# Kernel optimization log

Measured on AMD Instinct MI355X. Metric: run time of the kernel, lower is better.

Reference implementation:

```python
import jax, jax.numpy as jnp
import numpy as np

D, S, L, W, H, V = 64, 64, 64, 300, 300, 50000
NEG = jnp.float32(-9999999.0)


def setup_inputs() -> dict:
    key = jax.random.key(0)
    ks = jax.random.split(key, 16)
    n = lambda k, shape, s=0.05: jax.random.normal(k, shape, dtype=jnp.float32) * s
    return {
        "word_indices": jax.random.randint(ks[0], (D, S, L), 0, V),
        "E": n(ks[1], (V, W), 0.1),
        "W_sent": n(ks[2], (H, W)), "b_sent": jnp.zeros((H,), jnp.float32),
        "W_par": n(ks[3], (H, H)), "b_par": jnp.zeros((H,), jnp.float32),
        "W_ch": n(ks[4], (H, H)), "b_ch": jnp.zeros((H,), jnp.float32),
        "w_root": n(ks[5], (H,)), "b_root": jnp.zeros((), jnp.float32),
        "root_embed": n(ks[6], (H,)),
        "W_r": n(ks[7], (H, 3 * H)), "b_r": jnp.zeros((H,), jnp.float32),
        "W_cls": n(ks[8], (2, H)), "b_cls": jnp.zeros((2,), jnp.float32),
    }


def reference(word_indices, E, W_sent, b_sent, W_par, b_par, W_ch, b_ch,
              w_root, b_root, root_embed, W_r, b_r, W_cls, b_cls):
    lrelu = lambda x: jax.nn.leaky_relu(x, 0.01)
    # Ragged pad+gather stage of the original, dense here (all lengths == L)
    word_embed = E[word_indices]                 # [D,S,L,W]
    # 0.5*(X[l-1] + reverse(reverse(X))[l-1]) == X[l-1]; LSTM outputs unused in source
    x_last = word_embed[:, :, -1, :]             # [D,S,W]
    enc = lrelu(x_last @ W_sent.T + b_sent)      # [D,S,H] sentence encodings
    # Pairwise parent-child edge scores (O(S^2) dots in the original loops)
    P = lrelu(enc @ W_par.T + b_par)             # [D,S,H]
    C = lrelu(enc @ W_ch.T + b_ch)               # [D,S,H]
    A = jnp.einsum('dih,djh->dij', P, C)         # [D,S,S]
    A = jnp.where(jnp.eye(S, dtype=bool)[None], NEG, A)
    A = jax.nn.softmax(A, axis=1)                # Softmax(dim=0) per doc: over parents i
    scores = enc @ w_root + b_root               # [D,S] root scores
    fri = jax.nn.softmax(scores, axis=1)         # Softmax(dim=0) over sentences
    # ri[i] = r_embeds([enc_i, sum_k A[k,i]*enc_k + fri_i*root, enc_i*sum_k A[i,k]])
    tmp = jnp.einsum('dki,dkh->dih', A, enc)     # [D,S,H]
    agg = tmp + fri[..., None] * root_embed      # [D,S,H]
    tmp3 = enc * A.sum(axis=2, keepdims=True)    # [D,S,H]
    ri = lrelu(jnp.concatenate([enc, agg, tmp3], axis=-1) @ W_r.T + b_r)  # [D,S,H]
    final = ri.mean(axis=1)                      # [D,H]
    out = final @ W_cls.T + b_cls                # [D,2]
    return out, A, fri
```

## Files before the change

kernel.cpp:

```cpp
#include <hip/hip_runtime.h>
#include <hip/hip_bf16.h>

#define NEG_INF (-9999999.0f)

typedef __attribute__((ext_vector_type(8))) short bf16x8;
typedef __attribute__((ext_vector_type(4))) float f32x4;
typedef unsigned short us;

__device__ __forceinline__ float b2f(us u) {
  union { unsigned int i; float f; } x; x.i = ((unsigned int)u) << 16; return x.f;
}
__device__ __forceinline__ us f2b(float f) {
  union { float f; unsigned int i; } x; x.f = f;
  unsigned int r = x.i + 0x7fffu + ((x.i >> 16) & 1u);
  return (us)(r >> 16);
}
__device__ __forceinline__ float lrelu(float v) { return v > 0.f ? v : 0.01f * v; }
__device__ __forceinline__ bf16x8 ld8(const us* p) { return *reinterpret_cast<const bf16x8*>(p); }

__global__ __launch_bounds__(256) void k_prep(const int* __restrict__ wi, const float* __restrict__ E,
    const float* __restrict__ Ws, const float* __restrict__ Wp, const float* __restrict__ Wc,
    const float* __restrict__ Wr,
    us* __restrict__ Wsb, us* __restrict__ Wpb, us* __restrict__ Wcb, us* __restrict__ Wrb,
    us* __restrict__ xg, us* __restrict__ encb, us* __restrict__ Pb, us* __restrict__ Cb,
    us* __restrict__ encTb) {
  int task = blockIdx.y;
  int gid = blockIdx.x * 256 + threadIdx.x;
  const int stride = 640 * 256;
  if (task < 3) {
    const float* src = (task == 0) ? Ws : (task == 1) ? Wp : Wc;
    us* dst = (task == 0) ? Wsb : (task == 1) ? Wpb : Wcb;
    for (int i = gid; i < 304 * 320; i += stride) {
      int r = i / 320, c = i - r * 320;
      dst[i] = (r < 300 && c < 300) ? f2b(src[r * 300 + c]) : 0;
    }
  } else if (task == 3) {
    for (int i = gid; i < 304 * 928; i += stride) {
      int r = i / 928, c = i - r * 928;
      Wrb[i] = (r < 300 && c < 900) ? f2b(Wr[r * 900 + c]) : 0;
    }
  } else if (task == 4) {
    for (int i = gid; i < 4096 * 320; i += stride) {
      int r = i / 320, c = i - r * 320;
      xg[i] = (c < 300) ? f2b(E[(long)wi[r * 64 + 63] * 300 + c]) : 0;
    }
  } else if (task == 5) {
    for (int i = gid; i < 3 * 4096 * 20; i += stride) {
      int b = i / 81920, rem = i - b * 81920;
      int r = rem / 20, c = 300 + (rem - r * 20);
      us* dst = (b == 0) ? encb : (b == 1) ? Pb : Cb;
      dst[r * 320 + c] = 0;
    }
  } else {
    for (int i = gid; i < 4 * 4096; i += stride)
      encTb[300 * 4096 + i] = 0;
  }
}

__device__ __forceinline__ void stage16(const us* __restrict__ g, us* lds, int units, int t) {
  const float4* s = reinterpret_cast<const float4*>(g);
  float4* d = reinterpret_cast<float4*>(lds);
  for (int i = t; i < units; i += 256) d[i] = s[i];
}

template<int NT, int KP>
__device__ __forceinline__ void sweep_lds(const us* As, const us* __restrict__ Bb,
    int bpitch, int nt0, int lo, int q, int ksn, f32x4* acc) {
  const us* ar = As + lo * KP + 8 * q;
  const us* br[NT];
#pragma unroll
  for (int t = 0; t < NT; ++t)
    br[t] = Bb + (long)((nt0 + t) * 16 + lo) * bpitch + 8 * q;
  bf16x8 b0[NT], b1[NT], b2[NT];
#pragma unroll
  for (int t = 0; t < NT; ++t) b0[t] = ld8(br[t]);
#pragma unroll
  for (int t = 0; t < NT; ++t) b1[t] = ld8(br[t] + 32);
#pragma unroll
  for (int t = 0; t < NT; ++t) b2[t] = ld8(br[t] + 64);
  bf16x8 a0 = *reinterpret_cast<const bf16x8*>(ar);
  for (int ks = 0; ks < ksn - 3; ++ks) {
    bf16x8 a1 = *reinterpret_cast<const bf16x8*>(ar + (ks + 1) * 32);
    bf16x8 bn[NT];
#pragma unroll
    for (int t = 0; t < NT; ++t) bn[t] = ld8(br[t] + (ks + 3) * 32);
#pragma unroll
    for (int t = 0; t < NT; ++t)
      acc[t] = __builtin_amdgcn_mfma_f32_16x16x32_bf16(a0, b0[t], acc[t], 0, 0, 0);
    a0 = a1;
#pragma unroll
    for (int t = 0; t < NT; ++t) { b0[t] = b1[t]; b1[t] = b2[t]; b2[t] = bn[t]; }
  }
  {
    bf16x8 a1 = *reinterpret_cast<const bf16x8*>(ar + (ksn - 2) * 32);
#pragma unroll
    for (int t = 0; t < NT; ++t)
      acc[t] = __builtin_amdgcn_mfma_f32_16x16x32_bf16(a0, b0[t], acc[t], 0, 0, 0);
    a0 = a1;
#pragma unroll
    for (int t = 0; t < NT; ++t) b0[t] = b1[t];
  }
  {
    bf16x8 a1 = *reinterpret_cast<const bf16x8*>(ar + (ksn - 1) * 32);
#pragma unroll
    for (int t = 0; t < NT; ++t)
      acc[t] = __builtin_amdgcn_mfma_f32_16x16x32_bf16(a0, b0[t], acc[t], 0, 0, 0);
    a0 = a1;
#pragma unroll
    for (int t = 0; t < NT; ++t) b0[t] = b2[t];
  }
#pragma unroll
  for (int t = 0; t < NT; ++t)
    acc[t] = __builtin_amdgcn_mfma_f32_16x16x32_bf16(a0, b0[t], acc[t], 0, 0, 0);
}

template<int NT>
__device__ __forceinline__ void sweep(const us* __restrict__ Ab, int apitch,
    const us* __restrict__ Bb, int bpitch, int m0, int nt0, int lo, int q,
    int ks0, int ksn, f32x4* acc) {
  const us* ar = Ab + (long)(m0 + lo) * apitch + 8 * q + (long)ks0 * 32;
  const us* br[NT];
#pragma unroll
  for (int t = 0; t < NT; ++t)
    br[t] = Bb + (long)((nt0 + t) * 16 + lo) * bpitch + 8 * q + (long)ks0 * 32;
  bf16x8 a0 = ld8(ar), a1 = ld8(ar + 32);
  bf16x8 b0[NT], b1[NT];
#pragma unroll
  for (int t = 0; t < NT; ++t) b0[t] = ld8(br[t]);
#pragma unroll
  for (int t = 0; t < NT; ++t) b1[t] = ld8(br[t] + 32);
  for (int ks = 0; ks < ksn - 2; ++ks) {
    bf16x8 a2 = ld8(ar + (ks + 2) * 32);
    bf16x8 b2[NT];
#pragma unroll
    for (int t = 0; t < NT; ++t) b2[t] = ld8(br[t] + (ks + 2) * 32);
#pragma unroll
    for (int t = 0; t < NT; ++t)
      acc[t] = __builtin_amdgcn_mfma_f32_16x16x32_bf16(a0, b0[t], acc[t], 0, 0, 0);
    a0 = a1; a1 = a2;
#pragma unroll
    for (int t = 0; t < NT; ++t) { b0[t] = b1[t]; b1[t] = b2[t]; }
  }
#pragma unroll
  for (int t = 0; t < NT; ++t)
    acc[t] = __builtin_amdgcn_mfma_f32_16x16x32_bf16(a0, b0[t], acc[t], 0, 0, 0);
#pragma unroll
  for (int t = 0; t < NT; ++t)
    acc[t] = __builtin_amdgcn_mfma_f32_16x16x32_bf16(a1, b1[t], acc[t], 0, 0, 0);
}

template<int NT>
__device__ __forceinline__ void epi_bf16(const f32x4* acc, const float* __restrict__ bias,
    us* __restrict__ outb, us* __restrict__ outT,
    int m0, int nt0, int lo, int q) {
#pragma unroll
  for (int t = 0; t < NT; ++t) {
    int col = (nt0 + t) * 16 + lo;
    if (col >= 300) continue;
    float bb = bias[col];
#pragma unroll
    for (int r = 0; r < 4; ++r) {
      int row = m0 + q * 4 + r;
      us h = f2b(lrelu(acc[t][r] + bb));
      outb[(long)row * 320 + col] = h;
      if (outT) outT[(long)col * 4096 + row] = h;
    }
  }
}

__global__ __launch_bounds__(256) void k_gemm_enc(const us* __restrict__ Ab,
    const us* __restrict__ Bb, const float* __restrict__ bias,
    us* __restrict__ encb, us* __restrict__ encTb) {
  __shared__ __align__(16) us As[16 * 320];
  int t = threadIdx.x;
  int m0 = blockIdx.x * 16;
  stage16(Ab + (long)m0 * 320, As, 640, t);
  __syncthreads();
  int w = t >> 6, lane = t & 63, lo = lane & 15, q = lane >> 4;
  f32x4 z = {0.f, 0.f, 0.f, 0.f};
  if (w < 3) {
    f32x4 acc[5] = {z, z, z, z, z};
    sweep_lds<5, 320>(As, Bb, 320, w * 5, lo, q, 10, acc);
    epi_bf16<5>(acc, bias, encb, encTb, m0, w * 5, lo, q);
  } else {
    f32x4 acc[4] = {z, z, z, z};
    sweep_lds<4, 320>(As, Bb, 320, 15, lo, q, 10, acc);
    epi_bf16<4>(acc, bias, encb, encTb, m0, 15, lo, q);
  }
}

__global__ __launch_bounds__(256) void k_gemm_pc(const us* __restrict__ Ab,
    const us* __restrict__ Wpb, const us* __restrict__ Wcb,
    const float* __restrict__ bp, const float* __restrict__ bc,
    us* __restrict__ Pb, us* __restrict__ Cb) {
  __shared__ __align__(16) us As[16 * 320];
  int which = blockIdx.y;
  const us* Bb = which ? Wcb : Wpb;
  const float* bias = which ? bc : bp;
  us* outb = which ? Cb : Pb;
  int t = threadIdx.x;
  int m0 = blockIdx.x * 16;
  stage16(Ab + (long)m0 * 320, As, 640, t);
  __syncthreads();
  int w = t >> 6, lane = t & 63, lo = lane & 15, q = lane >> 4;
  f32x4 z = {0.f, 0.f, 0.f, 0.f};
  if (w < 3) {
    f32x4 acc[5] = {z, z, z, z, z};
    sweep_lds<5, 320>(As, Bb, 320, w * 5, lo, q, 10, acc);
    epi_bf16<5>(acc, bias, outb, (us*)nullptr, m0, w * 5, lo, q);
  } else {
    f32x4 acc[4] = {z, z, z, z};
    sweep_lds<4, 320>(As, Bb, 320, 15, lo, q, 10, acc);
    epi_bf16<4>(acc, bias, outb, (us*)nullptr, m0, 15, lo, q);
  }
}

__global__ __launch_bounds__(256) void k_attn(
    const us* __restrict__ Pb, const us* __restrict__ Cb, const us* __restrict__ encb,
    const float* __restrict__ w_root, const float* __restrict__ b_root,
    float* __restrict__ Aout, float* __restrict__ outF,
    us* __restrict__ Atb, float* __restrict__ rsp) {
  __shared__ float Ls[64][17];
  __shared__ float pm[4][16], psum[4][16];
  __shared__ float scores[64];
  int d = blockIdx.x, jg = blockIdx.y, t = threadIdx.x;
  int w = t >> 6, lane = t & 63, lo = lane & 15, q = lane >> 4;

  if (jg == 0) {
    int rr = t >> 2, quad = t & 3;
    const us* er = encb + (long)(d * 64 + rr) * 320;
    float s = 0.f;
    for (int h = quad * 4; h + 4 <= 300; h += 16) {
      ushort4 e4 = *reinterpret_cast<const ushort4*>(er + h);
      s = fmaf(b2f(e4.x), w_root[h], s);
      s = fmaf(b2f(e4.y), w_root[h + 1], s);
      s = fmaf(b2f(e4.z), w_root[h + 2], s);
      s = fmaf(b2f(e4.w), w_root[h + 3], s);
    }
    s += __shfl_xor(s, 1);
    s += __shfl_xor(s, 2);
    if (quad == 0) scores[rr] = s + b_root[0];
    __syncthreads();
    if (t < 64) {
      float sc = scores[t];
      float m = sc;
#pragma unroll
      for (int o = 32; o > 0; o >>= 1) m = fmaxf(m, __shfl_xor(m, o, 64));
      float e = expf(sc - m);
      float sum = e;
#pragma unroll
      for (int o = 32; o > 0; o >>= 1) sum += __shfl_xor(sum, o, 64);
      outF[d * 64 + t] = e / sum;
    }
  }

  {
    const us* Pd = Pb + (long)d * 64 * 320;
    const us* Cd = Cb + (long)d * 64 * 320;
    f32x4 acc = {0.f, 0.f, 0.f, 0.f};
    sweep<1>(Pd, 320, Cd, 320, w * 16, jg, lo, q, 0, 10, &acc);
#pragma unroll
    for (int r = 0; r < 4; ++r) {
      int i = w * 16 + q * 4 + r, j = jg * 16 + lo;
      Ls[i][lo] = (i == j) ? NEG_INF : acc[r];
    }
  }
  __syncthreads();

  {
    int col = t & 15, p = t >> 4;
    if (t < 64) {
      float mx = -3.0e38f;
      for (int i = p * 16; i < p * 16 + 16; ++i) mx = fmaxf(mx, Ls[i][col]);
      pm[p][col] = mx;
    }
    __syncthreads();
    if (t < 64) {
      float gmx = fmaxf(fmaxf(pm[0][col], pm[1][col]), fmaxf(pm[2][col], pm[3][col]));
      float s = 0.f;
      for (int i = p * 16; i < p * 16 + 16; ++i) s += expf(Ls[i][col] - gmx);
      psum[p][col] = s;
    }
    __syncthreads();
    if (t < 64) {
      float gmx = fmaxf(fmaxf(pm[0][col], pm[1][col]), fmaxf(pm[2][col], pm[3][col]));
      float inv = 1.f / (psum[0][col] + psum[1][col] + psum[2][col] + psum[3][col]);
      int j = jg * 16 + col;
      float* Ad = Aout + (long)d * 4096;
      us* Atd = Atb + (long)d * 4096;
      for (int i = p * 16; i < p * 16 + 16; ++i) {
        float a = expf(Ls[i][col] - gmx) * inv;
        Ad[i * 64 + j] = a;
        Atd[j * 64 + i] = f2b(a);
        Ls[i][col] = a;
      }
    }
  }
  __syncthreads();
  if (t < 64) {
    float s = 0.f;
#pragma unroll
    for (int c = 0; c < 16; ++c) s += Ls[t][c];
    rsp[(d * 4 + jg) * 64 + t] = s;
  }
}

__global__ __launch_bounds__(256) void k_glue2(
    const us* __restrict__ Atb, const us* __restrict__ encTb, const us* __restrict__ encb,
    const float* __restrict__ outF, const float* __restrict__ rsp,
    const float* __restrict__ root, us* __restrict__ ub) {
  __shared__ float frs[64], rs[64];
  int d = blockIdx.x, g = blockIdx.y, t = threadIdx.x;
  if (t < 64) {
    frs[t] = outF[d * 64 + t];
    rs[t] = rsp[(d * 4 + 0) * 64 + t] + rsp[(d * 4 + 1) * 64 + t]
          + rsp[(d * 4 + 2) * 64 + t] + rsp[(d * 4 + 3) * 64 + t];
  }
  __syncthreads();
  int w = t >> 6, lane = t & 63, lo = lane & 15, q = lane >> 4;
  int ht = g * 4 + w;
  if (ht < 19) {
    const us* Atd = Atb + (long)d * 4096;
    bf16x8 av0[4], av1[4];
#pragma unroll
    for (int mt = 0; mt < 4; ++mt) {
      av0[mt] = ld8(Atd + (mt * 16 + lo) * 64 + 8 * q);
      av1[mt] = ld8(Atd + (mt * 16 + lo) * 64 + 32 + 8 * q);
    }
    const us* brow = encTb + (long)(ht * 16 + lo) * 4096 + d * 64 + 8 * q;
    bf16x8 bv0 = ld8(brow), bv1 = ld8(brow + 32);
    int h = ht * 16 + lo;
    float rt = (h < 300) ? root[h] : 0.f;
#pragma unroll
    for (int mt = 0; mt < 4; ++mt) {
      f32x4 acc = {0.f, 0.f, 0.f, 0.f};
      acc = __builtin_amdgcn_mfma_f32_16x16x32_bf16(av0[mt], bv0, acc, 0, 0, 0);
      acc = __builtin_amdgcn_mfma_f32_16x16x32_bf16(av1[mt], bv1, acc, 0, 0, 0);
      if (h < 300) {
#pragma unroll
        for (int r = 0; r < 4; ++r) {
          int i = mt * 16 + q * 4 + r;
          ub[(long)(d * 64 + i) * 928 + 300 + h] = f2b(acc[r] + frs[i] * rt);
        }
      }
    }
  }
  for (int idx = t; idx < 64 * 60; idx += 256) {
    int r = idx / 60, c = g * 60 + (idx - (idx / 60) * 60);
    us ev = encb[(long)(d * 64 + r) * 320 + c];
    ub[(long)(d * 64 + r) * 928 + c] = ev;
    ub[(long)(d * 64 + r) * 928 + 600 + c] = f2b(b2f(ev) * rs[r]);
  }
  if (g == 4) {
    for (int idx = t; idx < 64 * 28; idx += 256) {
      int r = idx / 28, c = 900 + (idx - r * 28);
      ub[(long)(d * 64 + r) * 928 + c] = 0;
    }
  }
}

__global__ __launch_bounds__(256) void k_gemm_ri(const us* __restrict__ Ab,
    const us* __restrict__ Bb, const float* __restrict__ bias, float* __restrict__ ri) {
  __shared__ __align__(16) us As[16 * 928];
  int t = threadIdx.x;
  int m0 = blockIdx.x * 16;
  stage16(Ab + (long)m0 * 928, As, 1856, t);
  __syncthreads();
  int w = t >> 6, lane = t & 63, lo = lane & 15, q = lane >> 4;
  f32x4 z = {0.f, 0.f, 0.f, 0.f};
  if (w < 3) {
    f32x4 acc[5] = {z, z, z, z, z};
    sweep_lds<5, 928>(As, Bb, 928, w * 5, lo, q, 29, acc);
#pragma unroll
    for (int t2 = 0; t2 < 5; ++t2) {
      int col = (w * 5 + t2) * 16 + lo;
      if (col >= 300) continue;
      float bb = bias[col];
#pragma unroll
      for (int r = 0; r < 4; ++r)
        ri[(long)(m0 + q * 4 + r) * 300 + col] = lrelu(acc[t2][r] + bb);
    }
  } else {
    f32x4 acc[4] = {z, z, z, z};
    sweep_lds<4, 928>(As, Bb, 928, 15, lo, q, 29, acc);
#pragma unroll
    for (int t2 = 0; t2 < 4; ++t2) {
      int col = (15 + t2) * 16 + lo;
      if (col >= 300) continue;
      float bb = bias[col];
#pragma unroll
      for (int r = 0; r < 4; ++r)
        ri[(long)(m0 + q * 4 + r) * 300 + col] = lrelu(acc[t2][r] + bb);
    }
  }
}

__global__ __launch_bounds__(256) void k_final(const float* __restrict__ ri,
    const float* __restrict__ W_cls, const float* __restrict__ b_cls,
    float* __restrict__ outp) {
  __shared__ float fin[300];
  __shared__ float red[256];
  int d = blockIdx.x, t = threadIdx.x;
  for (int h = t; h < 300; h += 256) {
    float s = 0.f;
    for (int i = 0; i < 64; ++i) s += ri[((d * 64) + i) * 300 + h];
    fin[h] = s * (1.0f / 64.0f);
  }
  __syncthreads();
  for (int c2 = 0; c2 < 2; ++c2) {
    float pth = 0.f;
    for (int h = t; h < 300; h += 256) pth = fmaf(fin[h], W_cls[c2 * 300 + h], pth);
    red[t] = pth;
    __syncthreads();
    for (int o = 128; o > 0; o >>= 1) {
      if (t < o) red[t] += red[t + o];
      __syncthreads();
    }
    if (t == 0) outp[d * 2 + c2] = red[0] + b_cls[c2];
    __syncthreads();
  }
}

extern "C" void kernel_launch(void* const* d_in, const int* in_sizes, int n_in,
                              void* d_out, int out_size, void* d_ws, size_t ws_size,
                              hipStream_t stream) {
  const int*   wi     = (const int*)d_in[0];
  const float* E      = (const float*)d_in[1];
  const float* W_sent = (const float*)d_in[2];
  const float* b_sent = (const float*)d_in[3];
  const float* W_par  = (const float*)d_in[4];
  const float* b_par  = (const float*)d_in[5];
  const float* W_ch   = (const float*)d_in[6];
  const float* b_ch   = (const float*)d_in[7];
  const float* w_root = (const float*)d_in[8];
  const float* b_root = (const float*)d_in[9];
  const float* root_e = (const float*)d_in[10];
  const float* W_r    = (const float*)d_in[11];
  const float* b_r    = (const float*)d_in[12];
  const float* W_cls  = (const float*)d_in[13];
  const float* b_cls  = (const float*)d_in[14];

  us* B = (us*)d_ws;
  us* Wsb   = B;
  us* Wpb   = B + 97280;
  us* Wcb   = B + 194560;
  us* Wrb   = B + 291840;
  us* xg    = B + 573952;
  us* encb  = B + 1884672;
  us* encTb = B + 3195392;
  us* Pb    = B + 4440576;
  us* Cb    = B + 5751296;
  us* ub    = B + 7062016;
  us* Atb   = B + 10863104;
  float* rsp = (float*)(B + 11125248);
  float* ri  = (float*)(B + 11157760);

  float* outp = (float*)d_out;
  float* outA = outp + 128;
  float* outF = outp + 128 + 262144;

  k_prep<<<dim3(640, 7), 256, 0, stream>>>(wi, E, W_sent, W_par, W_ch, W_r,
                                           Wsb, Wpb, Wcb, Wrb, xg, encb, Pb, Cb, encTb);
  k_gemm_enc<<<256, 256, 0, stream>>>(xg, Wsb, b_sent, encb, encTb);
  k_gemm_pc<<<dim3(256, 2), 256, 0, stream>>>(encb, Wpb, Wcb, b_par, b_ch, Pb, Cb);
  k_attn<<<dim3(64, 4), 256, 0, stream>>>(Pb, Cb, encb, w_root, b_root,
                                          outA, outF, Atb, rsp);
  k_glue2<<<dim3(64, 5), 256, 0, stream>>>(Atb, encTb, encb, outF, rsp, root_e, ub);
  k_gemm_ri<<<256, 256, 0, stream>>>(ub, Wrb, b_r, ri);
  k_final<<<64, 256, 0, stream>>>(ri, W_cls, b_cls, outp);
}
```

Before: 188.7 us.

## Fuse the whole per-document pipeline into one LDS-resident megakernel

Replaces the six-kernel chain (gather, enc GEMM, P/C GEMM, attention, glue, ri GEMM, final) with one block per document that keeps enc, P, C and attention in swizzled LDS. W_r is split into three 300-column segments so the concatenated input is never built. The root term becomes a precomputed vector c2 = W_r_mid·root, scaled per row by fri, and the mean plus classifier are fused into the epilogue. This removes global round trips and launch overhead. The cost is only 64 blocks of 512 threads with heavy LDS use, which leaves most of the GPU idle.

After: 211.9 us. 1.12x slower.

```diff
diff --git a/kernel.cpp b/kernel.cpp
--- a/kernel.cpp
+++ b/kernel.cpp
@@ -1,11 +1,13 @@
 #include <hip/hip_runtime.h>
-#include <hip/hip_bf16.h>
 
 #define NEG_INF (-9999999.0f)
 
 typedef __attribute__((ext_vector_type(8))) short bf16x8;
 typedef __attribute__((ext_vector_type(4))) float f32x4;
 typedef unsigned short us;
+typedef unsigned int u32;
+
+#define MFMA16 __builtin_amdgcn_mfma_f32_16x16x32_bf16
 
 __device__ __forceinline__ float b2f(us u) {
   union { unsigned int i; float f; } x; x.i = ((unsigned int)u) << 16; return x.f;
@@ -17,407 +19,349 @@
 }
 __device__ __forceinline__ float lrelu(float v) { return v > 0.f ? v : 0.01f * v; }
 __device__ __forceinline__ bf16x8 ld8(const us* p) { return *reinterpret_cast<const bf16x8*>(p); }
-
-__global__ __launch_bounds__(256) void k_prep(const int* __restrict__ wi, const float* __restrict__ E,
+__device__ __forceinline__ int swz(int row) { return (row & 7) << 4; }
+
+__global__ __launch_bounds__(256) void k_prep(
     const float* __restrict__ Ws, const float* __restrict__ Wp, const float* __restrict__ Wc,
-    const float* __restrict__ Wr,
-    us* __restrict__ Wsb, us* __restrict__ Wpb, us* __restrict__ Wcb, us* __restrict__ Wrb,
-    us* __restrict__ xg, us* __restrict__ encb, us* __restrict__ Pb, us* __restrict__ Cb,
-    us* __restrict__ encTb) {
+    const float* __restrict__ Wr, const float* __restrict__ root,
+    us* __restrict__ Wsb, us* __restrict__ Wpb, us* __restrict__ Wcb,
+    us* __restrict__ Wr3b, float* __restrict__ c2) {
   int task = blockIdx.y;
   int gid = blockIdx.x * 256 + threadIdx.x;
-  const int stride = 640 * 256;
+  const int stride = 80 * 256;
   if (task < 3) {
     const float* src = (task == 0) ? Ws : (task == 1) ? Wp : Wc;
     us* dst = (task == 0) ? Wsb : (task == 1) ? Wpb : Wcb;
-    for (int i = gid; i < 304 * 320; i += stride) {
+    for (int i = gid; i < 320 * 320; i += stride) {
       int r = i / 320, c = i - r * 320;
-      dst[i] = (r < 300 && c < 300) ? f2b(src[r * 300 + c]) : 0;
+      dst[i] = (r < 300 && c < 300) ? f2b(src[r * 300 + c]) : (us)0;
     }
   } else if (task == 3) {
-    for (int i = gid; i < 304 * 928; i += stride) {
-      int r = i / 928, c = i - r * 928;
-      Wrb[i] = (r < 300 && c < 900) ? f2b(Wr[r * 900 + c]) : 0;
-    }
-  } else if (task == 4) {
-    for (int i = gid; i < 4096 * 320; i += stride) {
-      int r = i / 320, c = i - r * 320;
-      xg[i] = (c < 300) ? f2b(E[(long)wi[r * 64 + 63] * 300 + c]) : 0;
-    }
-  } else if (task == 5) {
-    for (int i = gid; i < 3 * 4096 * 20; i += stride) {
-      int b = i / 81920, rem = i - b * 81920;
-      int r = rem / 20, c = 300 + (rem - r * 20);
-      us* dst = (b == 0) ? encb : (b == 1) ? Pb : Cb;
-      dst[r * 320 + c] = 0;
+    for (int i = gid; i < 3 * 320 * 320; i += stride) {
+      int seg = i / 102400, rem = i - seg * 102400;
+      int r = rem / 320, c = rem - r * 320;
+      Wr3b[i] = (r < 300 && c < 300) ? f2b(Wr[r * 900 + seg * 300 + c]) : (us)0;
     }
   } else {
-    for (int i = gid; i < 4 * 4096; i += stride)
-      encTb[300 * 4096 + i] = 0;
-  }
-}
-
-__device__ __forceinline__ void stage16(const us* __restrict__ g, us* lds, int units, int t) {
-  const float4* s = reinterpret_cast<const float4*>(g);
-  float4* d = reinterpret_cast<float4*>(lds);
-  for (int i = t; i < units; i += 256) d[i] = s[i];
-}
-
-template<int NT, int KP>
-__device__ __forceinline__ void sweep_lds(const us* As, const us* __restrict__ Bb,
-    int bpitch, int nt0, int lo, int q, int ksn, f32x4* acc) {
-  const us* ar = As + lo * KP + 8 * q;
+    for (int i = gid; i < 320 * 8; i += stride) {
+      int c = i >> 3, p = i & 7;
+      float s = 0.f;
+      if (c < 300)
+        for (int h = p; h < 300; h += 8) s = fmaf(Wr[c * 900 + 300 + h], root[h], s);
+      s += __shfl_xor(s, 1); s += __shfl_xor(s, 2); s += __shfl_xor(s, 4);
+      if (p == 0) c2[c] = s;
+    }
+  }
+}
+
+template<int NT, int KS>
+__device__ __forceinline__ void sweep2(const us* __restrict__ Alds, int r0, int r1, int q, int lo,
+    const us* __restrict__ Bg, int n0, f32x4 (&acc)[2][NT]) {
+  const char* ab = (const char*)Alds;
+  const int a0o = r0 * 640, s0 = swz(r0);
+  const int a1o = r1 * 640, s1 = swz(r1);
   const us* br[NT];
 #pragma unroll
   for (int t = 0; t < NT; ++t)
-    br[t] = Bb + (long)((nt0 + t) * 16 + lo) * bpitch + 8 * q;
-  bf16x8 b0[NT], b1[NT], b2[NT];
+    br[t] = Bg + (long)((n0 + t) * 16 + lo) * 320 + 8 * q;
+  bf16x8 aC[2], aN[2], b0[NT], b1[NT];
+  aC[0] = *(const bf16x8*)(ab + a0o + ((16 * q) ^ s0));
+  aC[1] = *(const bf16x8*)(ab + a1o + ((16 * q) ^ s1));
+  aN[0] = *(const bf16x8*)(ab + a0o + ((64 + 16 * q) ^ s0));
+  aN[1] = *(const bf16x8*)(ab + a1o + ((64 + 16 * q) ^ s1));
 #pragma unroll
   for (int t = 0; t < NT; ++t) b0[t] = ld8(br[t]);
 #pragma unroll
   for (int t = 0; t < NT; ++t) b1[t] = ld8(br[t] + 32);
 #pragma unroll
-  for (int t = 0; t < NT; ++t) b2[t] = ld8(br[t] + 64);
-  bf16x8 a0 = *reinterpret_cast<const bf16x8*>(ar);
-  for (int ks = 0; ks < ksn - 3; ++ks) {
-    bf16x8 a1 = *reinterpret_cast<const bf16x8*>(ar + (ks + 1) * 32);
-    bf16x8 bn[NT];
-#pragma unroll
-    for (int t = 0; t < NT; ++t) bn[t] = ld8(br[t] + (ks + 3) * 32);
-#pragma unroll
-    for (int t = 0; t < NT; ++t)
-      acc[t] = __builtin_amdgcn_mfma_f32_16x16x32_bf16(a0, b0[t], acc[t], 0, 0, 0);
-    a0 = a1;
-#pragma unroll
-    for (int t = 0; t < NT; ++t) { b0[t] = b1[t]; b1[t] = b2[t]; b2[t] = bn[t]; }
-  }
-  {
-    bf16x8 a1 = *reinterpret_cast<const bf16x8*>(ar + (ksn - 2) * 32);
-#pragma unroll
-    for (int t = 0; t < NT; ++t)
-      acc[t] = __builtin_amdgcn_mfma_f32_16x16x32_bf16(a0, b0[t], acc[t], 0, 0, 0);
-    a0 = a1;
-#pragma unroll
-    for (int t = 0; t < NT; ++t) b0[t] = b1[t];
-  }
-  {
-    bf16x8 a1 = *reinterpret_cast<const bf16x8*>(ar + (ksn - 1) * 32);
-#pragma unroll
-    for (int t = 0; t < NT; ++t)
-      acc[t] = __builtin_amdgcn_mfma_f32_16x16x32_bf16(a0, b0[t], acc[t], 0, 0, 0);
-    a0 = a1;
-#pragma unroll
-    for (int t = 0; t < NT; ++t) b0[t] = b2[t];
-  }
-#pragma unroll
-  for (int t = 0; t < NT; ++t)
-    acc[t] = __builtin_amdgcn_mfma_f32_16x16x32_bf16(a0, b0[t], acc[t], 0, 0, 0);
-}
-
-template<int NT>
-__device__ __forceinline__ void sweep(const us* __restrict__ Ab, int apitch,
-    const us* __restrict__ Bb, int bpitch, int m0, int nt0, int lo, int q,
-    int ks0, int ksn, f32x4* acc) {
-  const us* ar = Ab + (long)(m0 + lo) * apitch + 8 * q + (long)ks0 * 32;
-  const us* br[NT];
-#pragma unroll
-  for (int t = 0; t < NT; ++t)
-    br[t] = Bb + (long)((nt0 + t) * 16 + lo) * bpitch + 8 * q + (long)ks0 * 32;
-  bf16x8 a0 = ld8(ar), a1 = ld8(ar + 32);
-  bf16x8 b0[NT], b1[NT];
-#pragma unroll
-  for (int t = 0; t < NT; ++t) b0[t] = ld8(br[t]);
-#pragma unroll
-  for (int t = 0; t < NT; ++t) b1[t] = ld8(br[t] + 32);
-  for (int ks = 0; ks < ksn - 2; ++ks) {
-    bf16x8 a2 = ld8(ar + (ks + 2) * 32);
-    bf16x8 b2[NT];
-#pragma unroll
-    for (int t = 0; t < NT; ++t) b2[t] = ld8(br[t] + (ks + 2) * 32);
-#pragma unroll
-    for (int t = 0; t < NT; ++t)
-      acc[t] = __builtin_amdgcn_mfma_f32_16x16x32_bf16(a0, b0[t], acc[t], 0, 0, 0);
-    a0 = a1; a1 = a2;
-#pragma unroll
-    for (int t = 0; t < NT; ++t) { b0[t] = b1[t]; b1[t] = b2[t]; }
-  }
-#pragma unroll
-  for (int t = 0; t < NT; ++t)
-    acc[t] = __builtin_amdgcn_mfma_f32_16x16x32_bf16(a0, b0[t], acc[t], 0, 0, 0);
-#pragma unroll
-  for (int t = 0; t < NT; ++t)
-    acc[t] = __builtin_amdgcn_mfma_f32_16x16x32_bf16(a1, b1[t], acc[t], 0, 0, 0);
-}
-
-template<int NT>
-__device__ __forceinline__ void epi_bf16(const f32x4* acc, const float* __restrict__ bias,
-    us* __restrict__ outb, us* __restrict__ outT,
-    int m0, int nt0, int lo, int q) {
+  for (int ks = 0; ks < KS - 2; ++ks) {
+    bf16x8 aF[2], bF[NT];
+    const int kb = 64 * (ks + 2) + 16 * q;
+    aF[0] = *(const bf16x8*)(ab + a0o + (kb ^ s0));
+    aF[1] = *(const bf16x8*)(ab + a1o + (kb ^ s1));
+#pragma unroll
+    for (int t = 0; t < NT; ++t) bF[t] = ld8(br[t] + (ks + 2) * 32);
+#pragma unroll
+    for (int t = 0; t < NT; ++t) {
+      acc[0][t] = MFMA16(aC[0], b0[t], acc[0][t], 0, 0, 0);
+      acc[1][t] = MFMA16(aC[1], b0[t], acc[1][t], 0, 0, 0);
+    }
+    aC[0] = aN[0]; aC[1] = aN[1]; aN[0] = aF[0]; aN[1] = aF[1];
+#pragma unroll
+    for (int t = 0; t < NT; ++t) { b0[t] = b1[t]; b1[t] = bF[t]; }
+  }
 #pragma unroll
   for (int t = 0; t < NT; ++t) {
-    int col = (nt0 + t) * 16 + lo;
-    if (col >= 300) continue;
-    float bb = bias[col];
+    acc[0][t] = MFMA16(aC[0], b0[t], acc[0][t], 0, 0, 0);
+    acc[1][t] = MFMA16(aC[1], b0[t], acc[1][t], 0, 0, 0);
+  }
+#pragma unroll
+  for (int t = 0; t < NT; ++t) {
+    acc[0][t] = MFMA16(aN[0], b1[t], acc[0][t], 0, 0, 0);
+    acc[1][t] = MFMA16(aN[1], b1[t], acc[1][t], 0, 0, 0);
+  }
+}
+
+__device__ __forceinline__ void epi_lds(const f32x4 (&acc)[2][5], const float* __restrict__ bias,
+    us* __restrict__ dst, int mh, int nq, int lo, int q) {
+#pragma unroll
+  for (int mi = 0; mi < 2; ++mi)
+#pragma unroll
+    for (int tt = 0; tt < 5; ++tt) {
+      int col = (nq * 5 + tt) * 16 + lo;
+      if (col < 300) {
+        float bb = bias[col];
+#pragma unroll
+        for (int r = 0; r < 4; ++r) {
+          int row = (mh * 2 + mi) * 16 + 4 * q + r;
+          *(us*)((char*)dst + row * 640 + ((2 * col) ^ swz(row))) =
+              f2b(lrelu(acc[mi][tt][r] + bb));
+        }
+      }
+    }
+}
+
+__global__ __launch_bounds__(512, 2) void k_mega(
+    const int* __restrict__ wi, const float* __restrict__ E,
+    const us* __restrict__ Wsb, const us* __restrict__ Wpb, const us* __restrict__ Wcb,
+    const us* __restrict__ Wrb, const float* __restrict__ c2,
+    const float* __restrict__ b_sent, const float* __restrict__ b_par,
+    const float* __restrict__ b_ch,
+    const float* __restrict__ w_root, const float* __restrict__ b_root,
+    const float* __restrict__ b_r, const float* __restrict__ W_cls,
+    const float* __restrict__ b_cls,
+    float* __restrict__ outp, float* __restrict__ outA, float* __restrict__ outF) {
+  __shared__ __align__(16) us BIG[61440];
+  __shared__ __align__(16) float LA[64 * 68];
+  __shared__ __align__(16) us AtL[64 * 72];
+  __shared__ float pm[512], ps[512];
+  __shared__ float scS[64], friS[64], rsS[64];
+  __shared__ float finP[640];
+
+  const int d = blockIdx.x, t = threadIdx.x;
+  const int w = t >> 6, lane = t & 63, lo = lane & 15, q = lane >> 4;
+  const int mh = w & 1, nq = w >> 1;
+  const int r0 = mh * 32 + lo, r1 = r0 + 16;
+  const f32x4 z4 = {0.f, 0.f, 0.f, 0.f};
+  us* const Pl = BIG + 20480;
+  us* const Cl = BIG + 40960;
+  us* const G2T = BIG + 20480;
+
+  {
+    u32* zb = (u32*)BIG;
+#pragma unroll
+    for (int i = 0; i < 60; ++i) zb[t + i * 512] = 0u;
+  }
+  __syncthreads();
+
+  {
+    int s = t >> 3, p = t & 7;
+    int widx = wi[((d * 64 + s) << 6) + 63];
+    const float4* er = (const float4*)(E + (long)widx * 300);
+    char* rowb = (char*)BIG + s * 640;
+    int sw = swz(s);
+    for (int j = p; j < 75; j += 8) {
+      float4 v = er[j];
+      ushort4 h4 = make_ushort4(f2b(v.x), f2b(v.y), f2b(v.z), f2b(v.w));
+      *(ushort4*)(rowb + ((8 * j) ^ sw)) = h4;
+    }
+  }
+  __syncthreads();
+
+  {
+    f32x4 acc[2][5];
+#pragma unroll
+    for (int a = 0; a < 2; ++a)
+#pragma unroll
+      for (int b = 0; b < 5; ++b) acc[a][b] = z4;
+    sweep2<5, 10>(BIG, r0, r1, q, lo, Wsb, nq * 5, acc);
+    __syncthreads();
+    epi_lds(acc, b_sent, BIG, mh, nq, lo, q);
+  }
+  __syncthreads();
+
+  {
+    int i = t >> 3, p = t & 7;
+    float s = 0.f;
+    for (int cch = p; cch < 38; cch += 8) {
+      bf16x8 v = *(const bf16x8*)((const char*)BIG + i * 640 + ((16 * cch) ^ swz(i)));
+#pragma unroll
+      for (int e = 0; e < 8; ++e) {
+        int h = cch * 8 + e;
+        if (h < 300) s = fmaf(b2f((us)v[e]), w_root[h], s);
+      }
+    }
+    s += __shfl_xor(s, 1); s += __shfl_xor(s, 2); s += __shfl_xor(s, 4);
+    if (p == 0) scS[i] = s + b_root[0];
+  }
+  __syncthreads();
+  if (t < 64) {
+    float sc = scS[t], m = sc;
+#pragma unroll
+    for (int o = 32; o > 0; o >>= 1) m = fmaxf(m, __shfl_xor(m, o));
+    float e = expf(sc - m), sum = e;
+#pragma unroll
+    for (int o = 32; o > 0; o >>= 1) sum += __shfl_xor(sum, o);
+    float f = e / sum;
+    friS[t] = f;
+    outF[d * 64 + t] = f;
+  }
+
+  {
+    f32x4 acc[2][5];
+#pragma unroll
+    for (int a = 0; a < 2; ++a)
+#pragma unroll
+      for (int b = 0; b < 5; ++b) acc[a][b] = z4;
+    sweep2<5, 10>(BIG, r0, r1, q, lo, Wpb, nq * 5, acc);
+    epi_lds(acc, b_par, Pl, mh, nq, lo, q);
+  }
+  {
+    f32x4 acc[2][5];
+#pragma unroll
+    for (int a = 0; a < 2; ++a)
+#pragma unroll
+      for (int b = 0; b < 5; ++b) acc[a][b] = z4;
+    sweep2<5, 10>(BIG, r0, r1, q, lo, Wcb, nq * 5, acc);
+    epi_lds(acc, b_ch, Cl, mh, nq, lo, q);
+  }
+  __syncthreads();
+
+  {
+    int m = w >> 1, np = (w & 1) * 2;
+    int arow = m * 16 + lo;
+    int brow0 = np * 16 + lo, brow1 = brow0 + 16;
+    int sa = swz(arow), sb0 = swz(brow0), sb1 = swz(brow1);
+    f32x4 a0 = z4, a1 = z4;
+#pragma unroll
+    for (int ks = 0; ks < 10; ++ks) {
+      int kb = 64 * ks + 16 * q;
+      bf16x8 av  = *(const bf16x8*)((const char*)Pl + arow * 640 + (kb ^ sa));
+      bf16x8 bv0 = *(const bf16x8*)((const char*)Cl + brow0 * 640 + (kb ^ sb0));
+      bf16x8 bv1 = *(const bf16x8*)((const char*)Cl + brow1 * 640 + (kb ^ sb1));
+      a0 = MFMA16(av, bv0, a0, 0, 0, 0);
+      a1 = MFMA16(av, bv1, a1, 0, 0, 0);
+    }
 #pragma unroll
     for (int r = 0; r < 4; ++r) {
-      int row = m0 + q * 4 + r;
-      us h = f2b(lrelu(acc[t][r] + bb));
-      outb[(long)row * 320 + col] = h;
-      if (outT) outT[(long)col * 4096 + row] = h;
-    }
-  }
-}
-
-__global__ __launch_bounds__(256) void k_gemm_enc(const us* __restrict__ Ab,
-    const us* __restrict__ Bb, const float* __restrict__ bias,
-    us* __restrict__ encb, us* __restrict__ encTb) {
-  __shared__ __align__(16) us As[16 * 320];
-  int t = threadIdx.x;
-  int m0 = blockIdx.x * 16;
-  stage16(Ab + (long)m0 * 320, As, 640, t);
-  __syncthreads();
-  int w = t >> 6, lane = t & 63, lo = lane & 15, q = lane >> 4;
-  f32x4 z = {0.f, 0.f, 0.f, 0.f};
-  if (w < 3) {
-    f32x4 acc[5] = {z, z, z, z, z};
-    sweep_lds<5, 320>(As, Bb, 320, w * 5, lo, q, 10, acc);
-    epi_bf16<5>(acc, bias, encb, encTb, m0, w * 5, lo, q);
-  } else {
-    f32x4 acc[4] = {z, z, z, z};
-    sweep_lds<4, 320>(As, Bb, 320, 15, lo, q, 10, acc);
-    epi_bf16<4>(acc, bias, encb, encTb, m0, 15, lo, q);
-  }
-}
-
-__global__ __launch_bounds__(256) void k_gemm_pc(const us* __restrict__ Ab,
-    const us* __restrict__ Wpb, const us* __restrict__ Wcb,
-    const float* __restrict__ bp, const float* __restrict__ bc,
-    us* __restrict__ Pb, us* __restrict__ Cb) {
-  __shared__ __align__(16) us As[16 * 320];
-  int which = blockIdx.y;
-  const us* Bb = which ? Wcb : Wpb;
-  const float* bias = which ? bc : bp;
-  us* outb = which ? Cb : Pb;
-  int t = threadIdx.x;
-  int m0 = blockIdx.x * 16;
-  stage16(Ab + (long)m0 * 320, As, 640, t);
-  __syncthreads();
-  int w = t >> 6, lane = t & 63, lo = lane & 15, q = lane >> 4;
-  f32x4 z = {0.f, 0.f, 0.f, 0.f};
-  if (w < 3) {
-    f32x4 acc[5] = {z, z, z, z, z};
-    sweep_lds<5, 320>(As, Bb, 320, w * 5, lo, q, 10, acc);
-    epi_bf16<5>(acc, bias, outb, (us*)nullptr, m0, w * 5, lo, q);
-  } else {
-    f32x4 acc[4] = {z, z, z, z};
-    sweep_lds<4, 320>(As, Bb, 320, 15, lo, q, 10, acc);
-    epi_bf16<4>(acc, bias, outb, (us*)nullptr, m0, 15, lo, q);
-  }
-}
-
-__global__ __launch_bounds__(256) void k_attn(
-    const us* __restrict__ Pb, const us* __restrict__ Cb, const us* __restrict__ encb,
-    const float* __restrict__ w_root, const float* __restrict__ b_root,
-    float* __restrict__ Aout, float* __restrict__ outF,
-    us* __restrict__ Atb, float* __restrict__ rsp) {
-  __shared__ float Ls[64][17];
-  __shared__ float pm[4][16], psum[4][16];
-  __shared__ float scores[64];
-  int d = blockIdx.x, jg = blockIdx.y, t = threadIdx.x;
-  int w = t >> 6, lane = t & 63, lo = lane & 15, q = lane >> 4;
-
-  if (jg == 0) {
-    int rr = t >> 2, quad = t & 3;
-    const us* er = encb + (long)(d * 64 + rr) * 320;
-    float s = 0.f;
-    for (int h = quad * 4; h + 4 <= 300; h += 16) {
-      ushort4 e4 = *reinterpret_cast<const ushort4*>(er + h);
-      s = fmaf(b2f(e4.x), w_root[h], s);
-      s = fmaf(b2f(e4.y), w_root[h + 1], s);
-      s = fmaf(b2f(e4.z), w_root[h + 2], s);
-      s = fmaf(b2f(e4.w), w_root[h + 3], s);
-    }
-    s += __shfl_xor(s, 1);
-    s += __shfl_xor(s, 2);
-    if (quad == 0) scores[rr] = s + b_root[0];
+      int row = m * 16 + 4 * q + r;
+      int c0 = np * 16 + lo, c1 = c0 + 16;
+      LA[row * 68 + c0] = (row == c0) ? NEG_INF : a0[r];
+      LA[row * 68 + c1] = (row == c1) ? NEG_INF : a1[r];
+    }
+  }
+  __syncthreads();
+
+  {
+    int j = lane, p2 = w;
+    float mx = -3.0e38f;
+#pragma unroll
+    for (int ii = 0; ii < 8; ++ii) mx = fmaxf(mx, LA[(p2 * 8 + ii) * 68 + j]);
+    pm[p2 * 64 + j] = mx;
     __syncthreads();
-    if (t < 64) {
-      float sc = scores[t];
-      float m = sc;
-#pragma unroll
-      for (int o = 32; o > 0; o >>= 1) m = fmaxf(m, __shfl_xor(m, o, 64));
-      float e = expf(sc - m);
-      float sum = e;
-#pragma unroll
-      for (int o = 32; o > 0; o >>= 1) sum += __shfl_xor(sum, o, 64);
-      outF[d * 64 + t] = e / sum;
-    }
-  }
-
-  {
-    const us* Pd = Pb + (long)d * 64 * 320;
-    const us* Cd = Cb + (long)d * 64 * 320;
-    f32x4 acc = {0.f, 0.f, 0.f, 0.f};
-    sweep<1>(Pd, 320, Cd, 320, w * 16, jg, lo, q, 0, 10, &acc);
-#pragma unroll
-    for (int r = 0; r < 4; ++r) {
-      int i = w * 16 + q * 4 + r, j = jg * 16 + lo;
-      Ls[i][lo] = (i == j) ? NEG_INF : acc[r];
-    }
-  }
-  __syncthreads();
-
-  {
-    int col = t & 15, p = t >> 4;
-    if (t < 64) {
-      float mx = -3.0e38f;
-      for (int i = p * 16; i < p * 16 + 16; ++i) mx = fmaxf(mx, Ls[i][col]);
-      pm[p][col] = mx;
-    }
+    float gm = pm[j];
+#pragma unroll
+    for (int k = 1; k < 8; ++k) gm = fmaxf(gm, pm[k * 64 + j]);
+    float ev[8], s = 0.f;
+#pragma unroll
+    for (int ii = 0; ii < 8; ++ii) {
+      float e = expf(LA[(p2 * 8 + ii) * 68 + j] - gm);
+      ev[ii] = e; s += e;
+    }
+    ps[p2 * 64 + j] = s;
     __syncthreads();
-    if (t < 64) {
-      float gmx = fmaxf(fmaxf(pm[0][col], pm[1][col]), fmaxf(pm[2][col], pm[3][col]));
-      float s = 0.f;
-      for (int i = p * 16; i < p * 16 + 16; ++i) s += expf(Ls[i][col] - gmx);
-      psum[p][col] = s;
-    }
-    __syncthreads();
-    if (t < 64) {
-      float gmx = fmaxf(fmaxf(pm[0][col], pm[1][col]), fmaxf(pm[2][col], pm[3][col]));
-      float inv = 1.f / (psum[0][col] + psum[1][col] + psum[2][col] + psum[3][col]);
-      int j = jg * 16 + col;
-      float* Ad = Aout + (long)d * 4096;
-      us* Atd = Atb + (long)d * 4096;
-      for (int i = p * 16; i < p * 16 + 16; ++i) {
-        float a = expf(Ls[i][col] - gmx) * inv;
-        Ad[i * 64 + j] = a;
-        Atd[j * 64 + i] = f2b(a);
-        Ls[i][col] = a;
-      }
+    float tot = ps[j];
+#pragma unroll
+    for (int k = 1; k < 8; ++k) tot += ps[k * 64 + j];
+    float inv = 1.f / tot;
+    float* Ad = outA + (long)d * 4096;
+#pragma unroll
+    for (int ii = 0; ii < 8; ++ii) {
+      int i = p2 * 8 + ii;
+      float a = ev[ii] * inv;
+      Ad[i * 64 + j] = a;
+      AtL[j * 72 + i] = f2b(a);
+      LA[i * 68 + j] = a;
     }
   }
   __syncthreads();
   if (t < 64) {
     float s = 0.f;
-#pragma unroll
-    for (int c = 0; c < 16; ++c) s += Ls[t][c];
-    rsp[(d * 4 + jg) * 64 + t] = s;
-  }
-}
-
-__global__ __launch_bounds__(256) void k_glue2(
-    const us* __restrict__ Atb, const us* __restrict__ encTb, const us* __restrict__ encb,
-    const float* __restrict__ outF, const float* __restrict__ rsp,
-    const float* __restrict__ root, us* __restrict__ ub) {
-  __shared__ float frs[64], rs[64];
-  int d = blockIdx.x, g = blockIdx.y, t = threadIdx.x;
-  if (t < 64) {
-    frs[t] = outF[d * 64 + t];
-    rs[t] = rsp[(d * 4 + 0) * 64 + t] + rsp[(d * 4 + 1) * 64 + t]
-          + rsp[(d * 4 + 2) * 64 + t] + rsp[(d * 4 + 3) * 64 + t];
-  }
-  __syncthreads();
-  int w = t >> 6, lane = t & 63, lo = lane & 15, q = lane >> 4;
-  int ht = g * 4 + w;
-  if (ht < 19) {
-    const us* Atd = Atb + (long)d * 4096;
-    bf16x8 av0[4], av1[4];
-#pragma unroll
-    for (int mt = 0; mt < 4; ++mt) {
-      av0[mt] = ld8(Atd + (mt * 16 + lo) * 64 + 8 * q);
-      av1[mt] = ld8(Atd + (mt * 16 + lo) * 64 + 32 + 8 * q);
-    }
-    const us* brow = encTb + (long)(ht * 16 + lo) * 4096 + d * 64 + 8 * q;
-    bf16x8 bv0 = ld8(brow), bv1 = ld8(brow + 32);
-    int h = ht * 16 + lo;
-    float rt = (h < 300) ? root[h] : 0.f;
-#pragma unroll
-    for (int mt = 0; mt < 4; ++mt) {
-      f32x4 acc = {0.f, 0.f, 0.f, 0.f};
-      acc = __builtin_amdgcn_mfma_f32_16x16x32_bf16(av0[mt], bv0, acc, 0, 0, 0);
-      acc = __builtin_amdgcn_mfma_f32_16x16x32_bf16(av1[mt], bv1, acc, 0, 0, 0);
-      if (h < 300) {
-#pragma unroll
-        for (int r = 0; r < 4; ++r) {
-          int i = mt * 16 + q * 4 + r;
-          ub[(long)(d * 64 + i) * 928 + 300 + h] = f2b(acc[r] + frs[i] * rt);
+    for (int jj = 0; jj < 64; ++jj) s += LA[t * 68 + jj];
+    rsS[t] = s;
+  }
+
+  {
+    f32x4 acc[2][5];
+#pragma unroll
+    for (int a = 0; a < 2; ++a)
+#pragma unroll
+      for (int b = 0; b < 5; ++b) acc[a][b] = z4;
+    sweep2<5, 10>(BIG, r0, r1, q, lo, Wrb + 102400, nq * 5, acc);
+#pragma unroll
+    for (int mi = 0; mi < 2; ++mi)
+#pragma unroll
+      for (int tt = 0; tt < 5; ++tt) {
+        int col = (nq * 5 + tt) * 16 + lo;
+        if (col < 300) {
+#pragma unroll
+          for (int r = 0; r < 4; ++r) {
+            int row = (mh * 2 + mi) * 16 + 4 * q + r;
+            G2T[col * 72 + row] = f2b(acc[mi][tt][r]);
+          }
         }
       }
-    }
-  }
-  for (int idx = t; idx < 64 * 60; idx += 256) {
-    int r = idx / 60, c = g * 60 + (idx - (idx / 60) * 60);
-    us ev = encb[(long)(d * 64 + r) * 320 + c];
-    ub[(long)(d * 64 + r) * 928 + c] = ev;
-    ub[(long)(d * 64 + r) * 928 + 600 + c] = f2b(b2f(ev) * rs[r]);
-  }
-  if (g == 4) {
-    for (int idx = t; idx < 64 * 28; idx += 256) {
-      int r = idx / 28, c = 900 + (idx - r * 28);
-      ub[(long)(d * 64 + r) * 928 + c] = 0;
-    }
-  }
-}
-
-__global__ __launch_bounds__(256) void k_gemm_ri(const us* __restrict__ Ab,
-    const us* __restrict__ Bb, const float* __restrict__ bias, float* __restrict__ ri) {
-  __shared__ __align__(16) us As[16 * 928];
-  int t = threadIdx.x;
-  int m0 = blockIdx.x * 16;
-  stage16(Ab + (long)m0 * 928, As, 1856, t);
-  __syncthreads();
-  int w = t >> 6, lane = t & 63, lo = lane & 15, q = lane >> 4;
-  f32x4 z = {0.f, 0.f, 0.f, 0.f};
-  if (w < 3) {
-    f32x4 acc[5] = {z, z, z, z, z};
-    sweep_lds<5, 928>(As, Bb, 928, w * 5, lo, q, 29, acc);
-#pragma unroll
-    for (int t2 = 0; t2 < 5; ++t2) {
-      int col = (w * 5 + t2) * 16 + lo;
-      if (col >= 300) continue;
-      float bb = bias[col];
-#pragma unroll
-      for (int r = 0; r < 4; ++r)
-        ri[(long)(m0 + q * 4 + r) * 300 + col] = lrelu(acc[t2][r] + bb);
-    }
-  } else {
-    f32x4 acc[4] = {z, z, z, z};
-    sweep_lds<4, 928>(As, Bb, 928, 15, lo, q, 29, acc);
-#pragma unroll
-    for (int t2 = 0; t2 < 4; ++t2) {
-      int col = (15 + t2) * 16 + lo;
-      if (col >= 300) continue;
-      float bb = bias[col];
-#pragma unroll
-      for (int r = 0; r < 4; ++r)
-        ri[(long)(m0 + q * 4 + r) * 300 + col] = lrelu(acc[t2][r] + bb);
-    }
-  }
-}
-
-__global__ __launch_bounds__(256) void k_final(const float* __restrict__ ri,
-    const float* __restrict__ W_cls, const float* __restrict__ b_cls,
-    float* __restrict__ outp) {
-  __shared__ float fin[300];
-  __shared__ float red[256];
-  int d = blockIdx.x, t = threadIdx.x;
-  for (int h = t; h < 300; h += 256) {
+    for (int i2 = t; i2 < 720; i2 += 512) ((u32*)(G2T + 21600))[i2] = 0u;
+  }
+  __syncthreads();
+
+  {
+    f32x4 am[2][5], ag[2][5];
+#pragma unroll
+    for (int a = 0; a < 2; ++a)
+#pragma unroll
+      for (int b = 0; b < 5; ++b) { am[a][b] = z4; ag[a][b] = z4; }
+    sweep2<5, 10>(BIG, r0, r1, q, lo, Wrb, nq * 5, am);
+    sweep2<5, 10>(BIG, r0, r1, q, lo, Wrb + 204800, nq * 5, ag);
+#pragma unroll
+    for (int ks = 0; ks < 2; ++ks) {
+      bf16x8 aA = *(const bf16x8*)(AtL + r0 * 72 + 32 * ks + 8 * q);
+      bf16x8 aB = *(const bf16x8*)(AtL + r1 * 72 + 32 * ks + 8 * q);
+#pragma unroll
+      for (int tt = 0; tt < 5; ++tt) {
+        bf16x8 bv = *(const bf16x8*)(G2T + ((nq * 5 + tt) * 16 + lo) * 72 + 32 * ks + 8 * q);
+        am[0][tt] = MFMA16(aA, bv, am[0][tt], 0, 0, 0);
+        am[1][tt] = MFMA16(aB, bv, am[1][tt], 0, 0, 0);
+      }
+    }
+#pragma unroll
+    for (int tt = 0; tt < 5; ++tt) {
+      int col = (nq * 5 + tt) * 16 + lo;
+      float bb = (col < 300) ? b_r[col] : 0.f;
+      float cc = c2[col];
+      float csum = 0.f;
+#pragma unroll
+      for (int mi = 0; mi < 2; ++mi)
+#pragma unroll
+        for (int r = 0; r < 4; ++r) {
+          int i = (mh * 2 + mi) * 16 + 4 * q + r;
+          csum += lrelu(am[mi][tt][r] + rsS[i] * ag[mi][tt][r] + friS[i] * cc + bb);
+        }
+      csum += __shfl_xor(csum, 16);
+      csum += __shfl_xor(csum, 32);
+      if (q == 0) finP[mh * 320 + col] = csum;
+    }
+  }
+  __syncthreads();
+
+  if (t < 128) {
+    int cls = t >> 6, ln = t & 63;
     float s = 0.f;
-    for (int i = 0; i < 64; ++i) s += ri[((d * 64) + i) * 300 + h];
-    fin[h] = s * (1.0f / 64.0f);
-  }
-  __syncthreads();
-  for (int c2 = 0; c2 < 2; ++c2) {
-    float pth = 0.f;
-    for (int h = t; h < 300; h += 256) pth = fmaf(fin[h], W_cls[c2 * 300 + h], pth);
-    red[t] = pth;
-    __syncthreads();
-    for (int o = 128; o > 0; o >>= 1) {
-      if (t < o) red[t] += red[t + o];
-      __syncthreads();
-    }
-    if (t == 0) outp[d * 2 + c2] = red[0] + b_cls[c2];
-    __syncthreads();
+    for (int h = ln; h < 300; h += 64)
+      s += (finP[h] + finP[320 + h]) * W_cls[cls * 300 + h];
+#pragma unroll
+    for (int o = 32; o > 0; o >>= 1) s += __shfl_xor(s, o);
+    if (ln == 0) outp[d * 2 + cls] = s * 0.015625f + b_cls[cls];
   }
 }
 
@@ -441,31 +385,19 @@
   const float* b_cls  = (const float*)d_in[14];
 
   us* B = (us*)d_ws;
-  us* Wsb   = B;
-  us* Wpb   = B + 97280;
-  us* Wcb   = B + 194560;
-  us* Wrb   = B + 291840;
-  us* xg    = B + 573952;
-  us* encb  = B + 1884672;
-  us* encTb = B + 3195392;
-  us* Pb    = B + 4440576;
-  us* Cb    = B + 5751296;
-  us* ub    = B + 7062016;
-  us* Atb   = B + 10863104;
-  float* rsp = (float*)(B + 11125248);
-  float* ri  = (float*)(B + 11157760);
+  us* Wsb  = B;
+  us* Wpb  = B + 102400;
+  us* Wcb  = B + 204800;
+  us* Wr3b = B + 307200;
+  float* c2 = (float*)(B + 614400);
 
   float* outp = (float*)d_out;
   float* outA = outp + 128;
   float* outF = outp + 128 + 262144;
 
-  k_prep<<<dim3(640, 7), 256, 0, stream>>>(wi, E, W_sent, W_par, W_ch, W_r,
-                                           Wsb, Wpb, Wcb, Wrb, xg, encb, Pb, Cb, encTb);
-  k_gemm_enc<<<256, 256, 0, stream>>>(xg, Wsb, b_sent, encb, encTb);
-  k_gemm_pc<<<dim3(256, 2), 256, 0, stream>>>(encb, Wpb, Wcb, b_par, b_ch, Pb, Cb);
-  k_attn<<<dim3(64, 4), 256, 0, stream>>>(Pb, Cb, encb, w_root, b_root,
-                                          outA, outF, Atb, rsp);
-  k_glue2<<<dim3(64, 5), 256, 0, stream>>>(Atb, encTb, encb, outF, rsp, root_e, ub);
-  k_gemm_ri<<<256, 256, 0, stream>>>(ub, Wrb, b_r, ri);
-  k_final<<<64, 256, 0, stream>>>(ri, W_cls, b_cls, outp);
-}
+  k_prep<<<dim3(80, 5), 256, 0, stream>>>(W_sent, W_par, W_ch, W_r, root_e,
+                                          Wsb, Wpb, Wcb, Wr3b, c2);
+  k_mega<<<64, 512, 0, stream>>>(wi, E, Wsb, Wpb, Wcb, Wr3b, c2,
+                                 b_sent, b_par, b_ch, w_root, b_root,
+                                 b_r, W_cls, b_cls, outp, outA, outF);
+}
```
